# Kernel tuning notes

Hardware: AMD Instinct MI355X
Metric: run time of the kernel (lower is better)

Reference implementation:

```python
import jax, jax.numpy as jnp
import numpy as np

B, S, E = 2, 2048, 1024
HID = 1024
HEADS = 16
EPS = 1e-5
SCALE = (E * 2) ** (-0.5)  # source uses input_data_dim*2


def setup_inputs() -> dict:
    key = jax.random.key(0)
    k1, k2, k3 = jax.random.split(key, 3)
    return {
        "x": jax.random.normal(k1, (B, S, E), dtype=jnp.float32),
        "ln_g": jnp.ones((E,), jnp.float32),
        "ln_b": jnp.zeros((E,), jnp.float32),
        "W1": jax.random.normal(k2, (E, 3 * HID), jnp.float32) * 0.02,
        "b1": jnp.zeros((3 * HID,), jnp.float32),
        "W2": jax.random.normal(k3, (HID, HID), jnp.float32) * 0.02,
        "b2": jnp.zeros((HID,), jnp.float32),
    }


def reference(x, ln_g, ln_b, W1, b1, W2, b2):
    # LayerNorm over last dim
    mu = jnp.mean(x, axis=-1, keepdims=True)
    var = jnp.mean(jnp.square(x - mu), axis=-1, keepdims=True)
    xn = (x - mu) * jax.lax.rsqrt(var + EPS) * ln_g + ln_b
    # QKV projection: [B,S,3*HID]
    qkv = jnp.einsum('bse,ef->bsf', xn, W1) + b1
    # Faithful to source: flat reshape to (heads, B, S, 3*HID/heads)
    qkv_heads = qkv.reshape(HEADS, B, S, -1)
    q, k, v = jnp.split(qkv_heads, 3, axis=-1)  # each [H,B,S,d]
    scores = jnp.einsum('hbse,hbSe->hbsS', q, k) * SCALE  # [H,B,S,S]
    att = jax.nn.softmax(scores, axis=-1)
    full_att = jnp.einsum('hbsS,hbSe->hbse', att, v)  # [H,B,S,d]
    full_att = full_att.reshape(B, S, -1)  # faithful flat reshape -> [B,S,HID]
    out = jnp.einsum('bsh,hk->bsk', full_att, W2) + b2
    return out
```

## Files before the change

### kernel.cpp

```cpp
#include <hip/hip_runtime.h>

typedef unsigned short u16;
typedef __bf16 bf16x8 __attribute__((ext_vector_type(8)));
typedef float f32x4 __attribute__((ext_vector_type(4)));
typedef float f32x16 __attribute__((ext_vector_type(16)));
typedef unsigned int u32x4 __attribute__((ext_vector_type(4)));
typedef int i32x2 __attribute__((ext_vector_type(2)));

static constexpr float SCALE2 = 0.022097086912079608f * 1.4426950408889634f;

__device__ __forceinline__ u16 f2b(float f) {
  union { float f; unsigned int i; } v; v.f = f;
  unsigned int r = v.i + 0x7fffu + ((v.i >> 16) & 1u);
  return (u16)(r >> 16);
}
__device__ __forceinline__ unsigned int pk2(float a, float b) {
#if __has_builtin(__builtin_amdgcn_cvt_pk_bf16_f32)
  auto v = __builtin_amdgcn_cvt_pk_bf16_f32(a, b);
  unsigned int u;
  __builtin_memcpy(&u, &v, 4);
  return u;
#else
  union { float f; unsigned int i; } x, y; x.f = a; y.f = b;
  return ((x.i + 0x8000u) >> 16) | ((y.i + 0x8000u) & 0xffff0000u);
#endif
}
__device__ __forceinline__ i32x2 plswap(unsigned int a, unsigned int b) {
#if __has_builtin(__builtin_amdgcn_permlane32_swap)
  return __builtin_amdgcn_permlane32_swap((int)a, (int)b, false, false);
#else
  int d = (int)a, s = (int)b;
  asm volatile("v_permlane32_swap_b32 %0, %1" : "+v"(d), "+v"(s));
  i32x2 r; r[0] = d; r[1] = s; return r;
#endif
}
__device__ __forceinline__ void async16(const u16* g, u16* l) {
  __builtin_amdgcn_global_load_lds((const __attribute__((address_space(1))) void*)g,
                                   (__attribute__((address_space(3))) void*)l,
                                   16, 0, 0);
}

__global__ __launch_bounds__(256) void pre_kernel(const float* __restrict__ x,
                                                  const float* __restrict__ lg,
                                                  const float* __restrict__ lb,
                                                  u16* __restrict__ xn,
                                                  const float* __restrict__ W1,
                                                  u16* __restrict__ W1T,
                                                  const float* __restrict__ W2,
                                                  u16* __restrict__ W2T) {
  __shared__ __align__(16) u16 smem[64 * 72];
  const int bx = blockIdx.x;
  const int t = threadIdx.x;
  if (bx < 1024) {
    const int w = t >> 6, lane = t & 63;
    const int row = bx * 4 + w;
    const float* xr = x + (size_t)row * 1024;
    float4 v[4];
    float s = 0.f, ss = 0.f;
#pragma unroll
    for (int k = 0; k < 4; k++) {
      v[k] = *(const float4*)(xr + k * 256 + lane * 4);
      s += v[k].x + v[k].y + v[k].z + v[k].w;
      ss += v[k].x * v[k].x + v[k].y * v[k].y + v[k].z * v[k].z + v[k].w * v[k].w;
    }
#pragma unroll
    for (int off = 32; off >= 1; off >>= 1) {
      s += __shfl_xor(s, off, 64);
      ss += __shfl_xor(ss, off, 64);
    }
    const float mu = s * (1.0f / 1024.0f);
    const float var = ss * (1.0f / 1024.0f) - mu * mu;
    const float inv = rsqrtf(var + 1e-5f);
#pragma unroll
    for (int k = 0; k < 4; k++) {
      float4 gg = *(const float4*)(lg + k * 256 + lane * 4);
      float4 bb = *(const float4*)(lb + k * 256 + lane * 4);
      ushort4 o;
      o.x = f2b((v[k].x - mu) * inv * gg.x + bb.x);
      o.y = f2b((v[k].y - mu) * inv * gg.y + bb.y);
      o.z = f2b((v[k].z - mu) * inv * gg.z + bb.z);
      o.w = f2b((v[k].w - mu) * inv * gg.w + bb.w);
      *(ushort4*)(xn + (size_t)row * 1024 + k * 256 + lane * 4) = o;
    }
    return;
  }
  const float* in;
  u16* out;
  int C, c0, r0;
  if (bx < 1024 + 768) {
    const int idx = bx - 1024;
    C = 3072; in = W1; out = W1T;
    c0 = (idx % 48) * 64; r0 = (idx / 48) * 64;
  } else {
    const int idx = bx - 1792;
    C = 1024; in = W2; out = W2T;
    c0 = (idx % 16) * 64; r0 = (idx / 16) * 64;
  }
  const int row = t >> 2, cseg = t & 3;
  for (int it = 0; it < 4; it++) {
    float4 v = *(const float4*)&in[(size_t)(r0 + row) * C + c0 + it * 16 + cseg * 4];
    ushort4 o;
    o.x = f2b(v.x); o.y = f2b(v.y); o.z = f2b(v.z); o.w = f2b(v.w);
    *(ushort4*)&smem[row * 72 + it * 16 + cseg * 4] = o;
  }
  __syncthreads();
  const int orow = t >> 2, ch = t & 3;
  u16 vals[16];
  for (int j = 0; j < 16; j++) vals[j] = smem[(ch * 16 + j) * 72 + orow];
  u16* dp = out + (size_t)(c0 + orow) * 1024 + r0 + ch * 16;
  *(uint4*)&dp[0] = *(uint4*)&vals[0];
  *(uint4*)&dp[8] = *(uint4*)&vals[8];
}

template <int MODE, int MT>
__global__ __launch_bounds__(256) void gemm_bt(const u16* __restrict__ A,
                                               const u16* __restrict__ Bt,
                                               const float* __restrict__ bias,
                                               float* __restrict__ C,
                                               int M, int N, int K, int nbx,
                                               u16* __restrict__ Qc,
                                               u16* __restrict__ Kc,
                                               u16* __restrict__ Vtmp) {
  __shared__ __align__(16) u16 SMEM[(MT + 128) * 64];
  u16* As = SMEM;
  u16* Bs = SMEM + MT * 64;
  const int nwg = gridDim.x, cpx = nwg >> 3;
  const int l0 = blockIdx.x;
  const int l2 = (l0 & 7) * cpx + (l0 >> 3);
  const int bx = l2 % nbx, by = l2 / nbx;
  const int m0 = by * MT, n0 = bx * 128;
  const int t = threadIdx.x, w = t >> 6, lane = t & 63;
  const int q = lane >> 4, l16 = lane & 15;
  const int wm = (w >> 1) * (MT / 2), wn = (w & 1) * 64;
  constexpr int NI = MT / 32;

  const int gchunk = (lane & 7) ^ ((lane >> 3) & 7);
  const u16* ap = A + (size_t)(m0 + w * 8 + (lane >> 3)) * K + gchunk * 8;
  const u16* bp = Bt + (size_t)(n0 + w * 8 + (lane >> 3)) * K + gchunk * 8;
  u16* lA = &As[w * 512];
  u16* lB = &Bs[w * 512];

  f32x4 acc[NI][4];
  const f32x4 zero = {0.f, 0.f, 0.f, 0.f};
  for (int i = 0; i < NI; i++)
    for (int j = 0; j < 4; j++) acc[i][j] = zero;

  for (int k0 = 0; k0 < K; k0 += 64) {
    for (int i = 0; i < MT / 32; i++)
      async16(ap + (size_t)(i * 32) * K, lA + i * 2048);
    for (int i = 0; i < 4; i++)
      async16(bp + (size_t)(i * 32) * K, lB + i * 2048);
    ap += 64; bp += 64;
    __syncthreads();
    for (int kk = 0; kk < 2; kk++) {
      bf16x8 af[NI], bfr[4];
      for (int i = 0; i < NI; i++) {
        const int r = wm + i * 16 + l16;
        af[i] = *(const bf16x8*)&As[r * 64 + (((kk * 4 + q) ^ (r & 7)) * 8)];
      }
      for (int j = 0; j < 4; j++) {
        const int r = wn + j * 16 + l16;
        bfr[j] = *(const bf16x8*)&Bs[r * 64 + (((kk * 4 + q) ^ (r & 7)) * 8)];
      }
      for (int i = 0; i < NI; i++)
        for (int j = 0; j < 4; j++)
          acc[i][j] = __builtin_amdgcn_mfma_f32_16x16x32_bf16(af[i], bfr[j], acc[i][j], 0, 0, 0);
    }
    __syncthreads();
  }

  if constexpr (MODE == 0) {
    for (int j = 0; j < 4; j++) {
      const int col = n0 + wn + j * 16 + l16;
      const float bv = bias[col];
      for (int i = 0; i < NI; i++) {
        const int rbase = m0 + wm + i * 16 + q * 4;
        for (int r = 0; r < 4; r++)
          C[(size_t)(rbase + r) * N + col] = acc[i][j][r] + bv;
      }
    }
  } else {
    const int seg = n0 + wn;
    const int k64 = seg >> 6;
    const int tcol = k64 / 3;
    const int typ = k64 - tcol * 3;
    u16* dst = (typ == 0) ? Qc : (typ == 1) ? Kc : Vtmp;
    const float qs = (typ == 0) ? SCALE2 : 1.0f;
    const int gidx = m0 >> 7;
    u16* tw = &SMEM[w * 1280];
    float bv[4];
    for (int j = 0; j < 4; j++) bv[j] = bias[seg + j * 16 + l16];
    __syncthreads();
    for (int i = 0; i < 4; i++) {
      for (int j = 0; j < 4; j++) {
        ushort4 pk;
        pk.x = f2b((acc[i][j][0] + bv[j]) * qs);
        pk.y = f2b((acc[i][j][1] + bv[j]) * qs);
        pk.z = f2b((acc[i][j][2] + bv[j]) * qs);
        pk.w = f2b((acc[i][j][3] + bv[j]) * qs);
        *(ushort4*)&tw[(j * 16 + l16) * 20 + q * 4] = pk;
      }
      const int r2 = lane >> 2;
      const int quarter = lane & 3;
      u16 vals[16];
      for (int c = 0; c < 16; c++)
        vals[c] = tw[(quarter * 16 + c) * 20 + r2];
      const int lr = wm + i * 16 + r2;
      const int s = (lr << 4) + tcol;
      u16* dp = dst + ((size_t)gidx * 2048 + s) * 64 + quarter * 16;
      *(uint4*)&dp[0] = *(uint4*)&vals[0];
      *(uint4*)&dp[8] = *(uint4*)&vals[8];
    }
  }
}

__global__ __launch_bounds__(256) void vtrans(const u16* __restrict__ Vtmp,
                                              u16* __restrict__ Vt) {
  __shared__ __align__(16) u16 tile[64 * 64];
  const int g = blockIdx.y, s0 = blockIdx.x * 64;
  const int t = threadIdx.x;
  const int row = t >> 3, ch = t & 7;
  for (int p = 0; p < 2; p++) {
    const int r = p * 32 + row;
    uint4 v = *(const uint4*)&Vtmp[((size_t)g * 2048 + s0 + r) * 64 + ch * 8];
    *(uint4*)&tile[r * 64 + ((ch ^ (r & 7)) * 8)] = v;
  }
  __syncthreads();
  const int d = t >> 2, scn = t & 3;
  u16 vals[16];
  for (int j2 = 0; j2 < 16; j2++) {
    const int s = scn * 16 + j2;
    vals[j2] = tile[s * 64 + (((d >> 3) ^ (s & 7)) * 8) + (d & 7)];
  }
  u16* dp = Vt + ((size_t)g * 64 + d) * 2048 + s0 + scn * 16;
  *(uint4*)&dp[0] = *(uint4*)&vals[0];
  *(uint4*)&dp[8] = *(uint4*)&vals[8];
}

__global__ __launch_bounds__(512) void attn_kernel(const u16* __restrict__ Qc,
                                                   const u16* __restrict__ Kc,
                                                   const u16* __restrict__ Vt,
                                                   u16* __restrict__ Oc) {
  __shared__ __align__(16) u16 LDS[25600];
  u16* K0 = LDS;
  u16* K1 = LDS + 4096;
  u16* V0 = LDS + 8192;
  u16* V1 = LDS + 12288;
  const int g = blockIdx.y;
  const int q0 = blockIdx.x * 128;
  const int t = threadIdx.x, w = t >> 6, lane = t & 63;
  const int l31 = lane & 31, h = lane >> 5;
  const int qs = w & 3;
  const int kvb = (w >> 2) * 32;

  const u16* Qg = Qc + (size_t)g * 2048 * 64;
  const u16* Kg = Kc + (size_t)g * 2048 * 64;
  const u16* Vg = Vt + (size_t)g * 64 * 2048;

  bf16x8 aq[4];
#pragma unroll
  for (int s = 0; s < 4; s++)
    aq[s] = *(const bf16x8*)&Qg[(size_t)(q0 + qs * 32 + l31) * 64 + s * 16 + h * 8];

  f32x16 accO[2];
#pragma unroll
  for (int tt = 0; tt < 2; tt++)
#pragma unroll
    for (int r = 0; r < 16; r++) accO[tt][r] = 0.f;
  float psv = 0.f;

  const int ch = (lane & 7) ^ ((lane >> 3) & 7);
  const u16* kp = Kg + (size_t)(w * 8 + (lane >> 3)) * 64 + ch * 8;
  const u16* vp = Vg + (size_t)(w * 8 + (lane >> 3)) * 2048 + ch * 8;
  u16* lK0 = K0 + w * 512;
  u16* lK1 = K1 + w * 512;
  u16* lV0 = V0 + w * 512;
  u16* lV1 = V1 + w * 512;

  const int rsw = l31 & 7;

  async16(kp, lK0);
  async16(vp, lV0);
  __syncthreads();

  for (int it = 0; it < 32; it++) {
    const int cur = it & 1;
    const u16* Kcur = cur ? K1 : K0;
    const u16* Vcur = cur ? V1 : V0;
    if (it < 31) {
      const int kt0 = (it + 1) * 64;
      async16(kp + (size_t)kt0 * 64, cur ? lK0 : lK1);
      async16(vp + kt0, cur ? lV0 : lV1);
    }

    f32x16 sa;
#pragma unroll
    for (int r = 0; r < 16; r++) sa[r] = 0.f;
    __builtin_amdgcn_s_setprio(1);
#pragma unroll
    for (int s = 0; s < 4; s++) {
      bf16x8 ak = *(const bf16x8*)&Kcur[(kvb + l31) * 64 + (((s * 2 + h) ^ rsw) * 8)];
      sa = __builtin_amdgcn_mfma_f32_32x32x16_bf16(ak, aq[s], sa, 0, 0, 0);
    }
    __builtin_amdgcn_s_setprio(0);

    float e[16];
#pragma unroll
    for (int r = 0; r < 16; r++) e[r] = __builtin_amdgcn_exp2f(sa[r]);
    psv += (((e[0] + e[1]) + (e[2] + e[3])) + ((e[4] + e[5]) + (e[6] + e[7])))
         + (((e[8] + e[9]) + (e[10] + e[11])) + ((e[12] + e[13]) + (e[14] + e[15])));
    unsigned int c[8];
#pragma unroll
    for (int m = 0; m < 8; m++) c[m] = pk2(e[2 * m], e[2 * m + 1]);
    i32x2 r02 = plswap(c[0], c[2]);
    i32x2 r13 = plswap(c[1], c[3]);
    i32x2 r46 = plswap(c[4], c[6]);
    i32x2 r57 = plswap(c[5], c[7]);
    bf16x8 pf[2];
    u32x4 f0 = {(unsigned)r02[0], (unsigned)r13[0], (unsigned)r02[1], (unsigned)r13[1]};
    u32x4 f1 = {(unsigned)r46[0], (unsigned)r57[0], (unsigned)r46[1], (unsigned)r57[1]};
    __builtin_memcpy(&pf[0], &f0, 16);
    __builtin_memcpy(&pf[1], &f1, 16);

    __builtin_amdgcn_s_setprio(1);
#pragma unroll
    for (int s = 0; s < 2; s++) {
#pragma unroll
      for (int tt = 0; tt < 2; tt++) {
        bf16x8 av = *(const bf16x8*)&Vcur[(tt * 32 + l31) * 64 + ((((kvb >> 3) + s * 2 + h) ^ rsw) * 8)];
        accO[tt] = __builtin_amdgcn_mfma_f32_32x32x16_bf16(av, pf[s], accO[tt], 0, 0, 0);
      }
    }
    __builtin_amdgcn_s_setprio(0);

    __syncthreads();
  }

  float* Red = (float*)LDS;
  if (w >= 4) {
    const int base = (w - 4) * 2048;
#pragma unroll
    for (int tt = 0; tt < 2; tt++)
#pragma unroll
      for (int m = 0; m < 4; m++) {
        f32x4 v4 = {accO[tt][4 * m], accO[tt][4 * m + 1], accO[tt][4 * m + 2], accO[tt][4 * m + 3]};
        *(f32x4*)&Red[base + (tt * 4 + m) * 256 + lane * 4] = v4;
      }
    Red[8192 + (w - 4) * 64 + lane] = psv;
  }
  __syncthreads();
  if (w < 4) {
#pragma unroll
    for (int tt = 0; tt < 2; tt++)
#pragma unroll
      for (int m = 0; m < 4; m++) {
        f32x4 v4 = *(const f32x4*)&Red[w * 2048 + (tt * 4 + m) * 256 + lane * 4];
        accO[tt][4 * m + 0] += v4[0];
        accO[tt][4 * m + 1] += v4[1];
        accO[tt][4 * m + 2] += v4[2];
        accO[tt][4 * m + 3] += v4[3];
      }
    psv += Red[8192 + w * 64 + lane];
    psv += __shfl_xor(psv, 32, 64);
    const float linv = 1.0f / psv;
    const int srow = q0 + qs * 32 + l31;
    const int orow = g * 128 + (srow >> 4);
    const int cbase = (srow & 15) * 64;
#pragma unroll
    for (int tt = 0; tt < 2; tt++)
#pragma unroll
      for (int m = 0; m < 4; m++) {
        ushort4 o;
        o.x = f2b(accO[tt][4 * m + 0] * linv);
        o.y = f2b(accO[tt][4 * m + 1] * linv);
        o.z = f2b(accO[tt][4 * m + 2] * linv);
        o.w = f2b(accO[tt][4 * m + 3] * linv);
        *(ushort4*)&Oc[(size_t)orow * 1024 + cbase + tt * 32 + m * 8 + h * 4] = o;
      }
  }
}

extern "C" void kernel_launch(void* const* d_in, const int* in_sizes, int n_in,
                              void* d_out, int out_size, void* d_ws, size_t ws_size,
                              hipStream_t stream) {
  (void)in_sizes; (void)n_in; (void)out_size; (void)ws_size;
  const float* x    = (const float*)d_in[0];
  const float* ln_g = (const float*)d_in[1];
  const float* ln_b = (const float*)d_in[2];
  const float* W1   = (const float*)d_in[3];
  const float* b1   = (const float*)d_in[4];
  const float* W2   = (const float*)d_in[5];
  const float* b2   = (const float*)d_in[6];

  char* ws = (char*)d_ws;
  u16* xn   = (u16*)(ws);
  u16* W1T  = (u16*)(ws + ((size_t)8 << 20));
  u16* W2T  = (u16*)(ws + ((size_t)14 << 20));
  u16* Qc   = (u16*)(ws + ((size_t)16 << 20));
  u16* Kc   = (u16*)(ws + ((size_t)24 << 20));
  u16* Vtmp = (u16*)(ws + ((size_t)32 << 20));
  u16* Vt   = (u16*)(ws + ((size_t)40 << 20));
  u16* Oc   = xn;

  pre_kernel<<<dim3(2048), dim3(256), 0, stream>>>(x, ln_g, ln_b, xn, W1, W1T, W2, W2T);
  gemm_bt<1, 128><<<dim3(768), dim3(256), 0, stream>>>(xn, W1T, b1, nullptr,
                                                       4096, 3072, 1024, 24, Qc, Kc, Vtmp);
  vtrans<<<dim3(32, 32), dim3(256), 0, stream>>>(Vtmp, Vt);
  attn_kernel<<<dim3(16, 32), dim3(512), 0, stream>>>(Qc, Kc, Vt, Oc);
  gemm_bt<0, 64><<<dim3(512), dim3(256), 0, stream>>>(Oc, W2T, b2, (float*)d_out,
                                                      4096, 1024, 1024, 8, nullptr, nullptr, nullptr);
}
```

Baseline: 187.5 us.

## Double KV tile size in attention loop to halve barriers per pass

The attention kernel now stages 128 keys/values per iteration instead of 64, doubling the LDS K/V buffers and running 16 iterations, each with two inner 64-key sub-steps. V tiles use a 128-wide row stride with a new swizzle, and each thread issues two async copies per operand. This is meant to halve the number of block barriers and prefetch issue points, amortising sync overhead over more MFMA work. In exchange it uses more shared memory per block, which could reduce occupancy.

```diff
diff --git a/kernel.cpp b/kernel.cpp
--- a/kernel.cpp
+++ b/kernel.cpp
@@ -241,11 +241,11 @@
                                                    const u16* __restrict__ Kc,
                                                    const u16* __restrict__ Vt,
                                                    u16* __restrict__ Oc) {
-  __shared__ __align__(16) u16 LDS[25600];
+  __shared__ __align__(16) u16 LDS[33792];
   u16* K0 = LDS;
-  u16* K1 = LDS + 4096;
-  u16* V0 = LDS + 8192;
-  u16* V1 = LDS + 12288;
+  u16* K1 = LDS + 8192;
+  u16* V0 = LDS + 16384;
+  u16* V1 = LDS + 24576;
   const int g = blockIdx.y;
   const int q0 = blockIdx.x * 128;
   const int t = threadIdx.x, w = t >> 6, lane = t & 63;
@@ -269,69 +269,89 @@
     for (int r = 0; r < 16; r++) accO[tt][r] = 0.f;
   float psv = 0.f;
 
-  const int ch = (lane & 7) ^ ((lane >> 3) & 7);
-  const u16* kp = Kg + (size_t)(w * 8 + (lane >> 3)) * 64 + ch * 8;
-  const u16* vp = Vg + (size_t)(w * 8 + (lane >> 3)) * 2048 + ch * 8;
-  u16* lK0 = K0 + w * 512;
-  u16* lK1 = K1 + w * 512;
-  u16* lV0 = V0 + w * 512;
-  u16* lV1 = V1 + w * 512;
+  const int kr = w * 16 + (lane >> 3);
+  const u16* kp = Kg + (size_t)kr * 64 + (((lane & 7) ^ (kr & 7)) * 8);
+  const int vd0 = w * 8 + (lane >> 4);
+  const int vd1 = vd0 + 4;
+  const u16* vp0 = Vg + (size_t)vd0 * 2048 + (((lane & 15) ^ (vd0 & 7)) * 8);
+  const u16* vp1 = Vg + (size_t)vd1 * 2048 + (((lane & 15) ^ (vd1 & 7)) * 8);
+  u16* lK0 = K0 + w * 1024;
+  u16* lK1 = K1 + w * 1024;
+  u16* lV0 = V0 + w * 1024;
+  u16* lV1 = V1 + w * 1024;
 
   const int rsw = l31 & 7;
 
   async16(kp, lK0);
-  async16(vp, lV0);
+  async16(kp + 512, lK0 + 512);
+  async16(vp0, lV0);
+  async16(vp1, lV0 + 512);
   __syncthreads();
 
-  for (int it = 0; it < 32; it++) {
+  const u16* kpn = kp + 8192;
+  const u16* vpn0 = vp0 + 128;
+  const u16* vpn1 = vp1 + 128;
+
+#pragma unroll 2
+  for (int it = 0; it < 16; it++) {
     const int cur = it & 1;
     const u16* Kcur = cur ? K1 : K0;
     const u16* Vcur = cur ? V1 : V0;
-    if (it < 31) {
-      const int kt0 = (it + 1) * 64;
-      async16(kp + (size_t)kt0 * 64, cur ? lK0 : lK1);
-      async16(vp + kt0, cur ? lV0 : lV1);
-    }
-
-    f32x16 sa;
-#pragma unroll
-    for (int r = 0; r < 16; r++) sa[r] = 0.f;
-    __builtin_amdgcn_s_setprio(1);
-#pragma unroll
-    for (int s = 0; s < 4; s++) {
-      bf16x8 ak = *(const bf16x8*)&Kcur[(kvb + l31) * 64 + (((s * 2 + h) ^ rsw) * 8)];
-      sa = __builtin_amdgcn_mfma_f32_32x32x16_bf16(ak, aq[s], sa, 0, 0, 0);
-    }
-    __builtin_amdgcn_s_setprio(0);
-
-    float e[16];
-#pragma unroll
-    for (int r = 0; r < 16; r++) e[r] = __builtin_amdgcn_exp2f(sa[r]);
-    psv += (((e[0] + e[1]) + (e[2] + e[3])) + ((e[4] + e[5]) + (e[6] + e[7])))
-         + (((e[8] + e[9]) + (e[10] + e[11])) + ((e[12] + e[13]) + (e[14] + e[15])));
-    unsigned int c[8];
-#pragma unroll
-    for (int m = 0; m < 8; m++) c[m] = pk2(e[2 * m], e[2 * m + 1]);
-    i32x2 r02 = plswap(c[0], c[2]);
-    i32x2 r13 = plswap(c[1], c[3]);
-    i32x2 r46 = plswap(c[4], c[6]);
-    i32x2 r57 = plswap(c[5], c[7]);
-    bf16x8 pf[2];
-    u32x4 f0 = {(unsigned)r02[0], (unsigned)r13[0], (unsigned)r02[1], (unsigned)r13[1]};
-    u32x4 f1 = {(unsigned)r46[0], (unsigned)r57[0], (unsigned)r46[1], (unsigned)r57[1]};
-    __builtin_memcpy(&pf[0], &f0, 16);
-    __builtin_memcpy(&pf[1], &f1, 16);
-
-    __builtin_amdgcn_s_setprio(1);
-#pragma unroll
-    for (int s = 0; s < 2; s++) {
-#pragma unroll
-      for (int tt = 0; tt < 2; tt++) {
-        bf16x8 av = *(const bf16x8*)&Vcur[(tt * 32 + l31) * 64 + ((((kvb >> 3) + s * 2 + h) ^ rsw) * 8)];
-        accO[tt] = __builtin_amdgcn_mfma_f32_32x32x16_bf16(av, pf[s], accO[tt], 0, 0, 0);
-      }
-    }
-    __builtin_amdgcn_s_setprio(0);
+    if (it < 15) {
+      u16* Kn = cur ? lK0 : lK1;
+      u16* Vn = cur ? lV0 : lV1;
+      async16(kpn, Kn);
+      async16(kpn + 512, Kn + 512);
+      async16(vpn0, Vn);
+      async16(vpn1, Vn + 512);
+      kpn += 8192;
+      vpn0 += 128;
+      vpn1 += 128;
+    }
+
+#pragma unroll
+    for (int hv = 0; hv < 2; hv++) {
+      f32x16 sa;
+#pragma unroll
+      for (int r = 0; r < 16; r++) sa[r] = 0.f;
+      __builtin_amdgcn_s_setprio(1);
+#pragma unroll
+      for (int s = 0; s < 4; s++) {
+        bf16x8 ak = *(const bf16x8*)&Kcur[(hv * 64 + kvb + l31) * 64 + (((s * 2 + h) ^ rsw) * 8)];
+        sa = __builtin_amdgcn_mfma_f32_32x32x16_bf16(ak, aq[s], sa, 0, 0, 0);
+      }
+      __builtin_amdgcn_s_setprio(0);
+
+      float e[16];
+#pragma unroll
+      for (int r = 0; r < 16; r++) e[r] = __builtin_amdgcn_exp2f(sa[r]);
+      psv += (((e[0] + e[1]) + (e[2] + e[3])) + ((e[4] + e[5]) + (e[6] + e[7])))
+           + (((e[8] + e[9]) + (e[10] + e[11])) + ((e[12] + e[13]) + (e[14] + e[15])));
+      unsigned int c[8];
+#pragma unroll
+      for (int m = 0; m < 8; m++) c[m] = pk2(e[2 * m], e[2 * m + 1]);
+      i32x2 r02 = plswap(c[0], c[2]);
+      i32x2 r13 = plswap(c[1], c[3]);
+      i32x2 r46 = plswap(c[4], c[6]);
+      i32x2 r57 = plswap(c[5], c[7]);
+      bf16x8 pf[2];
+      u32x4 f0 = {(unsigned)r02[0], (unsigned)r13[0], (unsigned)r02[1], (unsigned)r13[1]};
+      u32x4 f1 = {(unsigned)r46[0], (unsigned)r57[0], (unsigned)r46[1], (unsigned)r57[1]};
+      __builtin_memcpy(&pf[0], &f0, 16);
+      __builtin_memcpy(&pf[1], &f1, 16);
+
+      __builtin_amdgcn_s_setprio(1);
+#pragma unroll
+      for (int s = 0; s < 2; s++) {
+#pragma unroll
+        for (int tt = 0; tt < 2; tt++) {
+          bf16x8 av = *(const bf16x8*)&Vcur[(tt * 32 + l31) * 128 +
+                                            (((hv * 8 + (kvb >> 3) + s * 2 + h) ^ rsw) * 8)];
+          accO[tt] = __builtin_amdgcn_mfma_f32_32x32x16_bf16(av, pf[s], accO[tt], 0, 0, 0);
+        }
+      }
+      __builtin_amdgcn_s_setprio(0);
+    }
 
     __syncthreads();
   }
```

After: 196.7 us. 4.9% more time.
